# Performance work log

Hardware: AMD Instinct MI355X
Metric: run time of the kernel (lower is better)

The kernel has to match this reference:

```python
import jax, jax.numpy as jnp
import numpy as np

N, E = 50000, 800000
IN_FEATS, H, F = 128, 2, 64
NEG_SLOPE = 0.2


def _gat_conv(x, W, attn_l, attn_r, bias, src, dst):
    """DGL-style GATConv. x:[N,IN], W:[H*F,IN], attn_l/attn_r:[H,F], bias:[H*F]. Returns [N,H,F]."""
    z = (x @ W.T).reshape(N, H, F)                      # node projections
    el = jnp.einsum('nhf,hf->nh', z, attn_l)            # [N,H]
    er = jnp.einsum('nhf,hf->nh', z, attn_r)            # [N,H]
    e = jax.nn.leaky_relu(el[src] + er[dst], NEG_SLOPE) # [E,H] edge logits
    # edge softmax over incoming edges of each destination node
    m = jax.ops.segment_max(e, dst, num_segments=N)     # [N,H]
    ex = jnp.exp(e - m[dst])
    s = jax.ops.segment_sum(ex, dst, num_segments=N)    # [N,H]
    alpha = ex / s[dst]                                 # [E,H]
    msg = alpha[:, :, None] * z[src]                    # [E,H,F]
    out = jax.ops.segment_sum(msg, dst, num_segments=N) # [N,H,F]
    return out + bias.reshape(1, H, F)


def setup_inputs() -> dict:
    key = jax.random.key(0)
    ks = jax.random.split(key, 10)
    x = jax.random.normal(ks[0], (N, IN_FEATS), dtype=jnp.float32)
    h = jax.random.normal(ks[1], (N, H, F), dtype=jnp.float32)
    src = jax.random.randint(ks[2], (E,), 0, N, dtype=jnp.int32)
    dst = jax.random.randint(ks[3], (E,), 0, N, dtype=jnp.int32)
    sc = 1.0 / np.sqrt(IN_FEATS)
    W = jax.random.normal(ks[4], (3, H * F, IN_FEATS), dtype=jnp.float32) * sc  # r,u,c fc weights
    attn_l = jax.random.normal(ks[5], (3, H, F), dtype=jnp.float32) * 0.1
    attn_r = jax.random.normal(ks[6], (3, H, F), dtype=jnp.float32) * 0.1
    conv_bias = jax.random.normal(ks[7], (3, H * F), dtype=jnp.float32) * 0.02
    gate_bias = jax.random.uniform(ks[8], (3, H, F), dtype=jnp.float32)  # torch.rand init
    return {"x": x, "h": h, "W": W, "attn_l": attn_l, "attn_r": attn_r,
            "conv_bias": conv_bias, "gate_bias": gate_bias, "src": src, "dst": dst}


def reference(x, h, W, attn_l, attn_r, conv_bias, gate_bias, src, dst):
    # r, u, c gates; each GATConv is applied to x (use_hidden=False branch)
    r = jax.nn.sigmoid(_gat_conv(x, W[0], attn_l[0], attn_r[0], conv_bias[0], src, dst) + gate_bias[0])
    u = jax.nn.sigmoid(_gat_conv(x, W[1], attn_l[1], attn_r[1], conv_bias[1], src, dst) + gate_bias[1])
    # note: original computes h_ = r*h but never uses it in this branch (dead code)
    c = jax.nn.sigmoid(_gat_conv(x, W[2], attn_l[2], attn_r[2], conv_bias[2], src, dst) + gate_bias[2])
    new_h = u * h + (1.0 - u) * c
    return new_h
```

## Files before the change

kernel.cpp:

```cpp
#include <hip/hip_runtime.h>
#include <hip/hip_bf16.h>
#include <math.h>

#define NN 50000
#define EE 800000
#define KIN 128
#define HFD 128
#define ZB 256
#define NB 196
#define GB2 1564
#define SB 782
#define CAP 64
#define TRS 132

typedef __bf16 bf16_t;
typedef __bf16 bf16x8 __attribute__((ext_vector_type(8)));
typedef float f32x2 __attribute__((ext_vector_type(2)));
typedef float f32x4 __attribute__((ext_vector_type(4)));
typedef unsigned short u16;
typedef unsigned int u32;
typedef unsigned char u8;

__device__ __forceinline__ float ldf(const void* p, size_t i, int isf32) {
    return isf32 ? ((const float*)p)[i] : (float)((const bf16_t*)p)[i];
}
__device__ __forceinline__ bf16x8 load8bf(const void* base, size_t off, int isf32) {
    if (isf32) {
        const float4* p = (const float4*)((const float*)base + off);
        float4 u = p[0], v = p[1];
        bf16x8 r;
        r[0] = (bf16_t)u.x; r[1] = (bf16_t)u.y; r[2] = (bf16_t)u.z; r[3] = (bf16_t)u.w;
        r[4] = (bf16_t)v.x; r[5] = (bf16_t)v.y; r[6] = (bf16_t)v.z; r[7] = (bf16_t)v.w;
        return r;
    }
    return *(const bf16x8*)((const bf16_t*)base + off);
}

__device__ __forceinline__ uint2 pack8fp8(bf16x8 v) {
    u32 lo = __builtin_amdgcn_cvt_pk_fp8_f32((float)v[0], (float)v[1], 0u, false);
    lo = __builtin_amdgcn_cvt_pk_fp8_f32((float)v[2], (float)v[3], lo, true);
    u32 hi = __builtin_amdgcn_cvt_pk_fp8_f32((float)v[4], (float)v[5], 0u, false);
    hi = __builtin_amdgcn_cvt_pk_fp8_f32((float)v[6], (float)v[7], hi, true);
    return make_uint2(lo, hi);
}

__global__ __launch_bounds__(256) void k_front(const unsigned short* __restrict__ xw,
                                               const void* __restrict__ W,
                                               const void* __restrict__ attn_l,
                                               const void* __restrict__ attn_r,
                                               int* __restrict__ deg,
                                               int* __restrict__ dflag,
                                               bf16_t* __restrict__ walv)
{
    const int b = blockIdx.x, tid = threadIdx.x;
    int i = b * 256 + tid;
    if (i < NN) deg[i] = 0;
    if (b > 8) return;

    __shared__ int cnt;
    if (tid == 0) cnt = 0;
    __syncthreads();
    int c = 0;
    for (int k = tid; k < 2048; k += 256) {
        int e = (xw[k] >> 7) & 0xFF;
        if (e > 150) c++;
    }
    atomicAdd(&cnt, c);
    __syncthreads();
    const int isf32 = (cnt > 20) ? 1 : 0;

    if (b == 0) {
        if (tid == 0) dflag[0] = isf32;
        return;
    }
    const int c8 = b - 1;
    const int side = c8 >> 2, g = (c8 >> 1) & 1, h = c8 & 1;
    const void* attn = side ? attn_r : attn_l;
    const int k = tid;
    if (k < KIN) {
        float acc = 0.f;
        for (int f = 0; f < 64; f++) {
            float wv = ldf(W, ((size_t)(g + 1) * HFD + h * 64 + f) * KIN + k, isf32);
            float av = ldf(attn, (size_t)((g + 1) * 2 + h) * 64 + f, isf32);
            acc += wv * av;
        }
        walv[(size_t)c8 * KIN + k] = (bf16_t)acc;
    }
}

__global__ __launch_bounds__(256) void k_big(const void* __restrict__ x,
                                             const void* __restrict__ W,
                                             const bf16_t* __restrict__ walv,
                                             u8* __restrict__ z8,
                                             float* __restrict__ eln,
                                             float* __restrict__ ern,
                                             const int* __restrict__ src,
                                             const int* __restrict__ dst,
                                             int* __restrict__ deg,
                                             u16* __restrict__ ssrc,
                                             const int* __restrict__ dflag)
{
    __shared__ bf16_t wlds[128 * 128];

    if (blockIdx.x >= GB2) {
        int base = (blockIdx.x - GB2) * 1024 + threadIdx.x * 4;
        if (base < EE) {
            int4 s4 = *(const int4*)(src + base);
            int4 d4 = *(const int4*)(dst + base);
            int p0 = atomicAdd(&deg[d4.x], 1);
            int p1 = atomicAdd(&deg[d4.y], 1);
            int p2 = atomicAdd(&deg[d4.z], 1);
            int p3 = atomicAdd(&deg[d4.w], 1);
            if (p0 < CAP) ssrc[d4.x * CAP + p0] = (u16)s4.x;
            if (p1 < CAP) ssrc[d4.y * CAP + p1] = (u16)s4.y;
            if (p2 < CAP) ssrc[d4.z * CAP + p2] = (u16)s4.z;
            if (p3 < CAP) ssrc[d4.w * CAP + p3] = (u16)s4.w;
        }
        return;
    }

    const int isf32 = dflag[0];
    const int tid = threadIdx.x;
    const int ng = blockIdx.x >> 1;
    const int g  = blockIdx.x & 1;

    for (int c = tid; c < 2048; c += 256) {
        int col = c >> 4, g8 = c & 15;
        bf16x8 v = load8bf(W, ((size_t)(g + 1) * HFD + col) * KIN + g8 * 8, isf32);
        *(bf16x8*)(wlds + (size_t)col * 128 + (g8 ^ (col & 15)) * 8) = v;
    }

    const int wave = tid >> 6;
    const int lane = tid & 63;
    const int quad = lane >> 4;
    const int lm   = lane & 15;
    const int node_base = ng * 64 + wave * 16;

    int nld = node_base + lm;
    if (nld > NN - 1) nld = NN - 1;

    bf16x8 a[4];
#pragma unroll
    for (int kk = 0; kk < 4; kk++)
        a[kk] = load8bf(x, (size_t)nld * KIN + kk * 32 + quad * 8, isf32);

    __syncthreads();

    f32x4 acc[8];
#pragma unroll
    for (int t = 0; t < 8; t++) {
        const int wc = t * 16 + lm;
        f32x4 a4 = {0.f, 0.f, 0.f, 0.f};
#pragma unroll
        for (int kk = 0; kk < 4; kk++) {
            bf16x8 b = *(const bf16x8*)(wlds + (size_t)wc * 128 + ((kk * 4 + quad) ^ lm) * 8);
            a4 = __builtin_amdgcn_mfma_f32_16x16x32_bf16(a[kk], b, a4, 0, 0, 0);
        }
        acc[t] = a4;
    }

    if (g == 0) {
        f32x4 sacc = {0.f, 0.f, 0.f, 0.f};
#pragma unroll
        for (int kk = 0; kk < 4; kk++) {
            bf16x8 b;
            if (lm < 8) b = *(const bf16x8*)(walv + (size_t)lm * KIN + kk * 32 + quad * 8);
            else {
#pragma unroll
                for (int jj = 0; jj < 8; jj++) b[jj] = (bf16_t)0.f;
            }
            sacc = __builtin_amdgcn_mfma_f32_16x16x32_bf16(a[kk], b, sacc, 0, 0, 0);
        }
#pragma unroll
        for (int r = 0; r < 4; r++) {
            int nn = node_base + quad * 4 + r;
            if (nn < NN) {
                if (lm < 4)      eln[(size_t)nn * 4 + lm] = sacc[r];
                else if (lm < 8) ern[(size_t)nn * 4 + (lm - 4)] = sacc[r];
            }
        }
    }

    __syncthreads();
#pragma unroll
    for (int t = 0; t < 8; t++) {
#pragma unroll
        for (int r = 0; r < 4; r++)
            wlds[(size_t)(wave * 16 + quad * 4 + r) * TRS + t * 16 + lm] = (bf16_t)acc[t][r];
    }
    __syncthreads();
#pragma unroll
    for (int q = 0; q < 4; q++) {
        int node64 = q * 16 + (tid >> 4);
        int chunk  = tid & 15;
        bf16x8 v = *(const bf16x8*)(wlds + (size_t)node64 * TRS + chunk * 8);
        uint2 u = pack8fp8(v);
        int node = ng * 64 + node64;
        if (node < NN)
            *(uint2*)(z8 + (size_t)node * ZB + g * 128 + chunk * 8) = u;
    }
}

__global__ __launch_bounds__(256) void k_agg(const u8* __restrict__ z8,
                                             const int* __restrict__ deg,
                                             const u16* __restrict__ ssrc,
                                             const float* __restrict__ eln,
                                             const float* __restrict__ ern,
                                             const void* __restrict__ conv_bias,
                                             const void* __restrict__ gate_bias,
                                             const void* __restrict__ hin,
                                             void* __restrict__ out,
                                             const int* __restrict__ dflag)
{
    const int isf32 = dflag[0];
    const int wave = threadIdx.x >> 6;
    const int lane = threadIdx.x & 63;
    const int j = lane >> 4;
    const int n = blockIdx.x * 4 + wave;
    if (n >= NN) return;
    int cnt = deg[n];
    if (cnt > CAP) cnt = CAP;
    const u16* row = ssrc + (size_t)n * CAP;
    const u32* row32 = (const u32*)row;
    const float erj = ern[(size_t)n * 4 + j];
    const u32 zoff = 4 * lane;

    float a0 = 0.f, a1 = 0.f, a2 = 0.f, a3 = 0.f, s = 0.f;
    int i = 0;
    for (; i + 8 <= cnt; i += 8) {
        u32 rr[4];
#pragma unroll
        for (int q = 0; q < 4; q++) rr[q] = row32[(i >> 1) + q];
        int sn[8];
#pragma unroll
        for (int q = 0; q < 4; q++) { sn[2*q] = rr[q] & 0xFFFF; sn[2*q+1] = rr[q] >> 16; }
        u32 zb[8];
#pragma unroll
        for (int q = 0; q < 8; q++)
            zb[q] = *(const u32*)(z8 + (size_t)sn[q] * ZB + zoff);
        float w[8];
#pragma unroll
        for (int q = 0; q < 8; q++) {
            float v = eln[(size_t)sn[q] * 4 + j] + erj;
            v = v > 0.f ? v : 0.2f * v;
            w[q] = __expf(v);
        }
#pragma unroll
        for (int q = 0; q < 8; q++) {
            f32x2 lo = __builtin_amdgcn_cvt_pk_f32_fp8(zb[q], false);
            f32x2 hi = __builtin_amdgcn_cvt_pk_f32_fp8(zb[q], true);
            a0 += w[q] * lo[0];
            a1 += w[q] * lo[1];
            a2 += w[q] * hi[0];
            a3 += w[q] * hi[1];
            s += w[q];
        }
    }
    if (i + 4 <= cnt) {
        u32 rr[2];
#pragma unroll
        for (int q = 0; q < 2; q++) rr[q] = row32[(i >> 1) + q];
        int sn[4];
#pragma unroll
        for (int q = 0; q < 2; q++) { sn[2*q] = rr[q] & 0xFFFF; sn[2*q+1] = rr[q] >> 16; }
        u32 zb[4];
#pragma unroll
        for (int q = 0; q < 4; q++)
            zb[q] = *(const u32*)(z8 + (size_t)sn[q] * ZB + zoff);
#pragma unroll
        for (int q = 0; q < 4; q++) {
            float v = eln[(size_t)sn[q] * 4 + j] + erj;
            v = v > 0.f ? v : 0.2f * v;
            float w = __expf(v);
            f32x2 lo = __builtin_amdgcn_cvt_pk_f32_fp8(zb[q], false);
            f32x2 hi = __builtin_amdgcn_cvt_pk_f32_fp8(zb[q], true);
            a0 += w * lo[0];
            a1 += w * lo[1];
            a2 += w * hi[0];
            a3 += w * hi[1];
            s += w;
        }
        i += 4;
    }
    for (; i < cnt; i++) {
        int sn = row[i];
        u32 zb = *(const u32*)(z8 + (size_t)sn * ZB + zoff);
        float v = eln[(size_t)sn * 4 + j] + erj;
        v = v > 0.f ? v : 0.2f * v;
        float w = __expf(v);
        f32x2 lo = __builtin_amdgcn_cvt_pk_f32_fp8(zb, false);
        f32x2 hi = __builtin_amdgcn_cvt_pk_f32_fp8(zb, true);
        a0 += w * lo[0];
        a1 += w * lo[1];
        a2 += w * hi[0];
        a3 += w * hi[1];
        s += w;
    }

    float inv = (cnt > 0) ? 1.f / fmaxf(s, 1e-30f) : 0.f;
    float o[4] = {a0 * inv, a1 * inv, a2 * inv, a3 * inv};

    float res[4];
    float hh[4];
    if (lane < 32) {
#pragma unroll
        for (int t = 0; t < 4; t++)
            hh[t] = ldf(hin, (size_t)n * HFD + 4 * lane + t, isf32);
    }
#pragma unroll
    for (int t = 0; t < 4; t++) {
        int c = 4 * lane + t;
        int gate = c >> 7;
        int cf = c & 127;
        int h = cf >> 6, f = cf & 63;
        float ob = ldf(conv_bias, (size_t)(gate + 1) * 128 + cf, isf32)
                 + ldf(gate_bias, (size_t)((gate + 1) * 2 + h) * 64 + f, isf32);
        float gv = 1.f / (1.f + __expf(-(o[t] + ob)));
        float other = __shfl(gv, lane ^ 32, 64);
        if (lane < 32)
            res[t] = gv * hh[t] + (1.f - gv) * other;
    }
    if (lane < 32) {
        if (isf32) {
            float4 v = {res[0], res[1], res[2], res[3]};
            *(float4*)((float*)out + (size_t)n * HFD + 4 * lane) = v;
        } else {
            bf16_t v[4];
            v[0] = (bf16_t)res[0]; v[1] = (bf16_t)res[1];
            v[2] = (bf16_t)res[2]; v[3] = (bf16_t)res[3];
            *(uint2*)((bf16_t*)out + (size_t)n * HFD + 4 * lane) = *(uint2*)v;
        }
    }
}

extern "C" void kernel_launch(void* const* d_in, const int* in_sizes, int n_in,
                              void* d_out, int out_size, void* d_ws, size_t ws_size,
                              hipStream_t stream)
{
    const void* x         = d_in[0];
    const void* hin       = d_in[1];
    const void* W         = d_in[2];
    const void* attn_l    = d_in[3];
    const void* attn_r    = d_in[4];
    const void* conv_bias = d_in[5];
    const void* gate_bias = d_in[6];
    const int* src        = (const int*)d_in[7];
    const int* dst        = (const int*)d_in[8];

    char* p = (char*)d_ws;
    int* dflag    = (int*)p;    p += 256;
    u8* z8        = (u8*)p;     p += (size_t)NN * ZB;
    float* eln    = (float*)p;  p += (size_t)NN * 4 * 4;
    float* ern    = (float*)p;  p += (size_t)NN * 4 * 4;
    int* deg      = (int*)p;    p += (size_t)NN * 4;
    u16* ssrc     = (u16*)p;    p += (size_t)NN * CAP * 2;
    bf16_t* walv  = (bf16_t*)p; p += 8 * KIN * 2;

    k_front<<<NB, 256, 0, stream>>>((const unsigned short*)x, W, attn_l, attn_r,
                                    deg, dflag, walv);
    k_big<<<GB2 + SB, 256, 0, stream>>>(x, W, walv, z8, eln, ern, src, dst,
                                        deg, ssrc, dflag);
    k_agg<<<(NN + 3) / 4, 256, 0, stream>>>(z8, deg, ssrc, eln, ern,
                                            conv_bias, gate_bias, hin, d_out, dflag);
}
```

Measured before the change: 231.0 us.

## Shard edge bucketing per XCD to keep degree atomics local

The per-destination degree counters and source lists become eight replicas, one per XCD, chosen by reading the hardware XCC id. Scatter atomics from each XCD then hit only its own replica, which is meant to cut cross-die atomic contention and coherence traffic. The aggregation kernel merges the eight sub-lists into a per-wave shared-memory edge list using shuffles for prefix offsets. The cost is eight times more counters to zero and read, extra merge work per node, and a per-replica cap of 32 that can drop edges when one node's edges concentrate on a single XCD.

```diff
diff --git a/kernel.cpp b/kernel.cpp
--- a/kernel.cpp
+++ b/kernel.cpp
@@ -10,7 +10,8 @@
 #define NB 196
 #define GB2 1564
 #define SB 782
-#define CAP 64
+#define NR 8
+#define CAPR 32
 #define TRS 132
 
 typedef __bf16 bf16_t;
@@ -20,6 +21,12 @@
 typedef unsigned short u16;
 typedef unsigned int u32;
 typedef unsigned char u8;
+
+__device__ __forceinline__ int xcd_id() {
+    int x;
+    asm volatile("s_getreg_b32 %0, hwreg(HW_REG_XCC_ID)" : "=s"(x));
+    return x & (NR - 1);
+}
 
 __device__ __forceinline__ float ldf(const void* p, size_t i, int isf32) {
     return isf32 ? ((const float*)p)[i] : (float)((const bf16_t*)p)[i];
@@ -54,7 +61,10 @@
 {
     const int b = blockIdx.x, tid = threadIdx.x;
     int i = b * 256 + tid;
-    if (i < NN) deg[i] = 0;
+    if (i < NN) {
+#pragma unroll
+        for (int r = 0; r < NR; r++) deg[r * NN + i] = 0;
+    }
     if (b > 8) return;
 
     __shared__ int cnt;
@@ -103,18 +113,21 @@
     __shared__ bf16_t wlds[128 * 128];
 
     if (blockIdx.x >= GB2) {
+        const int r = xcd_id();
+        int* degr = deg + r * NN;
+        u16* ssr  = ssrc + (size_t)r * NN * CAPR;
         int base = (blockIdx.x - GB2) * 1024 + threadIdx.x * 4;
         if (base < EE) {
             int4 s4 = *(const int4*)(src + base);
             int4 d4 = *(const int4*)(dst + base);
-            int p0 = atomicAdd(&deg[d4.x], 1);
-            int p1 = atomicAdd(&deg[d4.y], 1);
-            int p2 = atomicAdd(&deg[d4.z], 1);
-            int p3 = atomicAdd(&deg[d4.w], 1);
-            if (p0 < CAP) ssrc[d4.x * CAP + p0] = (u16)s4.x;
-            if (p1 < CAP) ssrc[d4.y * CAP + p1] = (u16)s4.y;
-            if (p2 < CAP) ssrc[d4.z * CAP + p2] = (u16)s4.z;
-            if (p3 < CAP) ssrc[d4.w * CAP + p3] = (u16)s4.w;
+            int p0 = atomicAdd(&degr[d4.x], 1);
+            int p1 = atomicAdd(&degr[d4.y], 1);
+            int p2 = atomicAdd(&degr[d4.z], 1);
+            int p3 = atomicAdd(&degr[d4.w], 1);
+            if (p0 < CAPR) ssr[d4.x * CAPR + p0] = (u16)s4.x;
+            if (p1 < CAPR) ssr[d4.y * CAPR + p1] = (u16)s4.y;
+            if (p2 < CAPR) ssr[d4.z * CAPR + p2] = (u16)s4.z;
+            if (p3 < CAPR) ssr[d4.w * CAPR + p3] = (u16)s4.w;
         }
         return;
     }
@@ -212,25 +225,46 @@
                                              void* __restrict__ out,
                                              const int* __restrict__ dflag)
 {
+    __shared__ u16 elist_s[4][64];
     const int isf32 = dflag[0];
     const int wave = threadIdx.x >> 6;
     const int lane = threadIdx.x & 63;
     const int j = lane >> 4;
     const int n = blockIdx.x * 4 + wave;
-    if (n >= NN) return;
-    int cnt = deg[n];
-    if (cnt > CAP) cnt = CAP;
-    const u16* row = ssrc + (size_t)n * CAP;
-    const u32* row32 = (const u32*)row;
+    u16* elist = elist_s[wave];
+
+    const int r = lane >> 3, sub = lane & 7;
+    int cnt = deg[r * NN + n];
+    if (cnt > CAPR) cnt = CAPR;
+    int base = 0, tot = 0;
+#pragma unroll
+    for (int q = 0; q < 8; q++) {
+        int cq = __shfl(cnt, q * 8, 64);
+        if (q < r) base += cq;
+        tot += cq;
+    }
+    if (tot > 64) tot = 64;
+    const u16* ch = ssrc + ((size_t)r * NN + n) * CAPR;
+#pragma unroll
+    for (int t = 0; t < 4; t++) {
+        int idx = sub + t * 8;
+        if (idx < cnt) {
+            u16 v = ch[idx];
+            int d = base + idx;
+            if (d < 64) elist[d] = v;
+        }
+    }
+
     const float erj = ern[(size_t)n * 4 + j];
     const u32 zoff = 4 * lane;
+    const u32* el32 = (const u32*)elist;
 
     float a0 = 0.f, a1 = 0.f, a2 = 0.f, a3 = 0.f, s = 0.f;
     int i = 0;
-    for (; i + 8 <= cnt; i += 8) {
+    for (; i + 8 <= tot; i += 8) {
         u32 rr[4];
 #pragma unroll
-        for (int q = 0; q < 4; q++) rr[q] = row32[(i >> 1) + q];
+        for (int q = 0; q < 4; q++) rr[q] = el32[(i >> 1) + q];
         int sn[8];
 #pragma unroll
         for (int q = 0; q < 4; q++) { sn[2*q] = rr[q] & 0xFFFF; sn[2*q+1] = rr[q] >> 16; }
@@ -256,10 +290,10 @@
             s += w[q];
         }
     }
-    if (i + 4 <= cnt) {
+    if (i + 4 <= tot) {
         u32 rr[2];
 #pragma unroll
-        for (int q = 0; q < 2; q++) rr[q] = row32[(i >> 1) + q];
+        for (int q = 0; q < 2; q++) rr[q] = el32[(i >> 1) + q];
         int sn[4];
 #pragma unroll
         for (int q = 0; q < 2; q++) { sn[2*q] = rr[q] & 0xFFFF; sn[2*q+1] = rr[q] >> 16; }
@@ -282,8 +316,8 @@
         }
         i += 4;
     }
-    for (; i < cnt; i++) {
-        int sn = row[i];
+    for (; i < tot; i++) {
+        int sn = elist[i];
         u32 zb = *(const u32*)(z8 + (size_t)sn * ZB + zoff);
         float v = eln[(size_t)sn * 4 + j] + erj;
         v = v > 0.f ? v : 0.2f * v;
@@ -297,7 +331,7 @@
         s += w;
     }
 
-    float inv = (cnt > 0) ? 1.f / fmaxf(s, 1e-30f) : 0.f;
+    float inv = (tot > 0) ? 1.f / fmaxf(s, 1e-30f) : 0.f;
     float o[4] = {a0 * inv, a1 * inv, a2 * inv, a3 * inv};
 
     float res[4];
@@ -352,14 +386,14 @@
     u8* z8        = (u8*)p;     p += (size_t)NN * ZB;
     float* eln    = (float*)p;  p += (size_t)NN * 4 * 4;
     float* ern    = (float*)p;  p += (size_t)NN * 4 * 4;
-    int* deg      = (int*)p;    p += (size_t)NN * 4;
-    u16* ssrc     = (u16*)p;    p += (size_t)NN * CAP * 2;
+    int* deg      = (int*)p;    p += (size_t)NR * NN * 4;
+    u16* ssrc     = (u16*)p;    p += (size_t)NR * NN * CAPR * 2;
     bf16_t* walv  = (bf16_t*)p; p += 8 * KIN * 2;
 
     k_front<<<NB, 256, 0, stream>>>((const unsigned short*)x, W, attn_l, attn_r,
                                     deg, dflag, walv);
     k_big<<<GB2 + SB, 256, 0, stream>>>(x, W, walv, z8, eln, ern, src, dst,
                                         deg, ssrc, dflag);
-    k_agg<<<(NN + 3) / 4, 256, 0, stream>>>(z8, deg, ssrc, eln, ern,
-                                            conv_bias, gate_bias, hin, d_out, dflag);
-}
+    k_agg<<<NN / 4, 256, 0, stream>>>(z8, deg, ssrc, eln, ern,
+                                      conv_bias, gate_bias, hin, d_out, dflag);
+}
```

Result: slower. 245.3 us (+6.2%).

## Split each aggregation wave into two half-waves over interleaved edge chunks

Applied to the files above, without the earlier changes.

The aggregation kernel now splits each wave into two 32-lane halves. Each half takes a different 8-edge chunk of the destination's neighbor list, and each lane loads 8 fp8 features with a uint2 load instead of 4. The two halves' partial sums are combined with cross-lane shuffles. The remainder and tail loops are replaced by predicated masking with clamped indices. This doubles edge-level memory parallelism and widens loads, at the cost of wasted work on masked edges for low-degree nodes and extra shuffles in the epilogue.

```diff
diff --git a/kernel.cpp b/kernel.cpp
--- a/kernel.cpp
+++ b/kernel.cpp
@@ -215,120 +215,99 @@
     const int isf32 = dflag[0];
     const int wave = threadIdx.x >> 6;
     const int lane = threadIdx.x & 63;
-    const int j = lane >> 4;
+    const int half = lane >> 5;
+    const int sl   = lane & 31;
+    const int j    = sl >> 3;
     const int n = blockIdx.x * 4 + wave;
-    if (n >= NN) return;
     int cnt = deg[n];
     if (cnt > CAP) cnt = CAP;
-    const u16* row = ssrc + (size_t)n * CAP;
-    const u32* row32 = (const u32*)row;
+    const u32* row32 = (const u32*)(ssrc + (size_t)n * CAP);
     const float erj = ern[(size_t)n * 4 + j];
-    const u32 zoff = 4 * lane;
-
-    float a0 = 0.f, a1 = 0.f, a2 = 0.f, a3 = 0.f, s = 0.f;
-    int i = 0;
-    for (; i + 8 <= cnt; i += 8) {
+    const u32 zoff = sl * 8;
+
+    float acc[8] = {0.f, 0.f, 0.f, 0.f, 0.f, 0.f, 0.f, 0.f};
+    float s = 0.f;
+
+    for (int i = 0; i < cnt; i += 16) {
         u32 rr[4];
 #pragma unroll
-        for (int q = 0; q < 4; q++) rr[q] = row32[(i >> 1) + q];
+        for (int q = 0; q < 4; q++) rr[q] = row32[(i >> 1) + half * 4 + q];
         int sn[8];
-#pragma unroll
-        for (int q = 0; q < 4; q++) { sn[2*q] = rr[q] & 0xFFFF; sn[2*q+1] = rr[q] >> 16; }
-        u32 zb[8];
+        bool val[8];
+#pragma unroll
+        for (int q = 0; q < 8; q++) {
+            int v = (q & 1) ? (int)(rr[q >> 1] >> 16) : (int)(rr[q >> 1] & 0xFFFF);
+            val[q] = (i + half * 8 + q) < cnt;
+            sn[q] = (v < NN) ? v : 0;
+        }
+        uint2 zb[8];
 #pragma unroll
         for (int q = 0; q < 8; q++)
-            zb[q] = *(const u32*)(z8 + (size_t)sn[q] * ZB + zoff);
+            zb[q] = *(const uint2*)(z8 + (size_t)sn[q] * ZB + zoff);
         float w[8];
 #pragma unroll
         for (int q = 0; q < 8; q++) {
             float v = eln[(size_t)sn[q] * 4 + j] + erj;
             v = v > 0.f ? v : 0.2f * v;
-            w[q] = __expf(v);
+            float e = __expf(v);
+            w[q] = val[q] ? e : 0.f;
         }
 #pragma unroll
         for (int q = 0; q < 8; q++) {
-            f32x2 lo = __builtin_amdgcn_cvt_pk_f32_fp8(zb[q], false);
-            f32x2 hi = __builtin_amdgcn_cvt_pk_f32_fp8(zb[q], true);
-            a0 += w[q] * lo[0];
-            a1 += w[q] * lo[1];
-            a2 += w[q] * hi[0];
-            a3 += w[q] * hi[1];
+            f32x2 c01 = __builtin_amdgcn_cvt_pk_f32_fp8(zb[q].x, false);
+            f32x2 c23 = __builtin_amdgcn_cvt_pk_f32_fp8(zb[q].x, true);
+            f32x2 c45 = __builtin_amdgcn_cvt_pk_f32_fp8(zb[q].y, false);
+            f32x2 c67 = __builtin_amdgcn_cvt_pk_f32_fp8(zb[q].y, true);
+            acc[0] += w[q] * c01[0];
+            acc[1] += w[q] * c01[1];
+            acc[2] += w[q] * c23[0];
+            acc[3] += w[q] * c23[1];
+            acc[4] += w[q] * c45[0];
+            acc[5] += w[q] * c45[1];
+            acc[6] += w[q] * c67[0];
+            acc[7] += w[q] * c67[1];
             s += w[q];
         }
     }
-    if (i + 4 <= cnt) {
-        u32 rr[2];
-#pragma unroll
-        for (int q = 0; q < 2; q++) rr[q] = row32[(i >> 1) + q];
-        int sn[4];
-#pragma unroll
-        for (int q = 0; q < 2; q++) { sn[2*q] = rr[q] & 0xFFFF; sn[2*q+1] = rr[q] >> 16; }
-        u32 zb[4];
-#pragma unroll
-        for (int q = 0; q < 4; q++)
-            zb[q] = *(const u32*)(z8 + (size_t)sn[q] * ZB + zoff);
-#pragma unroll
-        for (int q = 0; q < 4; q++) {
-            float v = eln[(size_t)sn[q] * 4 + j] + erj;
-            v = v > 0.f ? v : 0.2f * v;
-            float w = __expf(v);
-            f32x2 lo = __builtin_amdgcn_cvt_pk_f32_fp8(zb[q], false);
-            f32x2 hi = __builtin_amdgcn_cvt_pk_f32_fp8(zb[q], true);
-            a0 += w * lo[0];
-            a1 += w * lo[1];
-            a2 += w * hi[0];
-            a3 += w * hi[1];
-            s += w;
-        }
-        i += 4;
-    }
-    for (; i < cnt; i++) {
-        int sn = row[i];
-        u32 zb = *(const u32*)(z8 + (size_t)sn * ZB + zoff);
-        float v = eln[(size_t)sn * 4 + j] + erj;
-        v = v > 0.f ? v : 0.2f * v;
-        float w = __expf(v);
-        f32x2 lo = __builtin_amdgcn_cvt_pk_f32_fp8(zb, false);
-        f32x2 hi = __builtin_amdgcn_cvt_pk_f32_fp8(zb, true);
-        a0 += w * lo[0];
-        a1 += w * lo[1];
-        a2 += w * hi[0];
-        a3 += w * hi[1];
-        s += w;
-    }
+
+#pragma unroll
+    for (int t = 0; t < 8; t++) acc[t] += __shfl(acc[t], lane ^ 32, 64);
+    s += __shfl(s, lane ^ 32, 64);
 
     float inv = (cnt > 0) ? 1.f / fmaxf(s, 1e-30f) : 0.f;
-    float o[4] = {a0 * inv, a1 * inv, a2 * inv, a3 * inv};
-
-    float res[4];
-    float hh[4];
-    if (lane < 32) {
-#pragma unroll
-        for (int t = 0; t < 4; t++)
-            hh[t] = ldf(hin, (size_t)n * HFD + 4 * lane + t, isf32);
-    }
-#pragma unroll
-    for (int t = 0; t < 4; t++) {
-        int c = 4 * lane + t;
+
+    float hh[8];
+    if (sl < 16) {
+#pragma unroll
+        for (int t = 0; t < 8; t++)
+            hh[t] = ldf(hin, (size_t)n * HFD + sl * 8 + t, isf32);
+    }
+    float res[8];
+#pragma unroll
+    for (int t = 0; t < 8; t++) {
+        int c = sl * 8 + t;
         int gate = c >> 7;
         int cf = c & 127;
         int h = cf >> 6, f = cf & 63;
         float ob = ldf(conv_bias, (size_t)(gate + 1) * 128 + cf, isf32)
                  + ldf(gate_bias, (size_t)((gate + 1) * 2 + h) * 64 + f, isf32);
-        float gv = 1.f / (1.f + __expf(-(o[t] + ob)));
-        float other = __shfl(gv, lane ^ 32, 64);
-        if (lane < 32)
+        float gv = 1.f / (1.f + __expf(-(acc[t] * inv + ob)));
+        float other = __shfl(gv, lane ^ 16, 64);
+        if (sl < 16)
             res[t] = gv * hh[t] + (1.f - gv) * other;
     }
-    if (lane < 32) {
+    if (lane < 16) {
         if (isf32) {
-            float4 v = {res[0], res[1], res[2], res[3]};
-            *(float4*)((float*)out + (size_t)n * HFD + 4 * lane) = v;
+            float4 v0 = {res[0], res[1], res[2], res[3]};
+            float4 v1 = {res[4], res[5], res[6], res[7]};
+            float* po = (float*)out + (size_t)n * HFD + lane * 8;
+            *(float4*)po = v0;
+            *(float4*)(po + 4) = v1;
         } else {
-            bf16_t v[4];
-            v[0] = (bf16_t)res[0]; v[1] = (bf16_t)res[1];
-            v[2] = (bf16_t)res[2]; v[3] = (bf16_t)res[3];
-            *(uint2*)((bf16_t*)out + (size_t)n * HFD + 4 * lane) = *(uint2*)v;
+            bf16_t v[8];
+#pragma unroll
+            for (int t = 0; t < 8; t++) v[t] = (bf16_t)res[t];
+            *(uint4*)((bf16_t*)out + (size_t)n * HFD + lane * 8) = *(uint4*)v;
         }
     }
 }
@@ -360,6 +339,6 @@
                                     deg, dflag, walv);
     k_big<<<GB2 + SB, 256, 0, stream>>>(x, W, walv, z8, eln, ern, src, dst,
                                         deg, ssrc, dflag);
-    k_agg<<<(NN + 3) / 4, 256, 0, stream>>>(z8, deg, ssrc, eln, ern,
-                                            conv_bias, gate_bias, hin, d_out, dflag);
-}
+    k_agg<<<NN / 4, 256, 0, stream>>>(z8, deg, ssrc, eln, ern,
+                                      conv_bias, gate_bias, hin, d_out, dflag);
+}
```

Result: slower. 320.0 us (+38.5%).
